# Performance work log

Measured on AMD Instinct MI355X. Metric: run time of the kernel, lower is better.

## Reference

```python
import jax, jax.numpy as jnp
import numpy as np

TEMP = 0.07
BASE_TEMP = 0.07
NUM_HEADS = 8


def setup_inputs() -> dict:
    key = jax.random.key(0)
    k1, k2, k3 = jax.random.split(key, 3)
    B, B2, V, E, C = 1024, 2048, 2, 512, 64
    features = jax.random.normal(k1, (B, V, E), dtype=jnp.float32)
    additional_negatives = jax.random.normal(k2, (B2, V, E), dtype=jnp.float32)
    labels = jax.random.bernoulli(k3, 0.05, (B, C)).astype(jnp.float32)
    return {"features": features, "additional_negatives": additional_negatives, "labels": labels}


def _l2norm(x, eps=1e-12):
    # matches torch.nn.functional.normalize (norm clamped at eps)
    n = jnp.linalg.norm(x, axis=-1, keepdims=True)
    return x / jnp.maximum(n, eps)


def reference(features, additional_negatives, labels):
    B, V, E = features.shape
    H = NUM_HEADS
    F = E // H
    N = B * V

    mask0 = (labels @ labels.T) > 0  # (B, B) label-overlap mask

    # torch.cat(torch.unbind(x, dim=1), dim=0): view-major concat -> (N, E)
    f = jnp.transpose(features, (1, 0, 2)).reshape(N, E).reshape(N, H, F)
    neg = jnp.transpose(additional_negatives, (1, 0, 2))
    M = neg.shape[0] * neg.shape[1]
    neg = neg.reshape(M, E // 1).reshape(M, H, F)

    f = _l2norm(f)
    neg = _l2norm(neg)

    # per-head pairwise similarities (the diagonal(dim1=2,dim2=3) of the full
    # (N,H,N,H) product keeps only matching heads -> einsum over shared h)
    D = jnp.einsum('ihf,jhf->ijh', f, f)      # (N, N, H)
    DN = jnp.einsum('ihf,mhf->imh', f, neg)   # (N, M, H)

    heads = jnp.argmax(D, axis=-1)            # (N, N) per-pair best head

    D = D / TEMP
    DN = DN / TEMP

    # The original builds L[i,k,j] = D[i,j,heads[i,k]]; its max over j and the
    # masked exp-sums depend only on (i, heads[i,k]), so compute per (i, h).
    m1 = jax.lax.stop_gradient(jnp.max(D, axis=1))   # (N, H) = max_j D[i,j,h]
    m2 = jax.lax.stop_gradient(jnp.max(DN, axis=1))  # (N, H) = max_m DN[i,m,h]

    not_self = 1.0 - jnp.eye(N, dtype=D.dtype)       # exclude j == i
    S1 = jnp.sum(jnp.exp(D - m1[:, None, :]) * not_self[:, :, None], axis=1)  # (N, H)
    S2 = jnp.sum(jnp.exp(DN - m2[:, None, :]), axis=1)                         # (N, H)

    # note: original sums exp terms referenced to DIFFERENT maxes (m1 vs m2);
    # reproduce that exactly.
    denom = m1 + jnp.log(S1 + S2)                    # (N, H)

    # diagonal term: D[i,k,heads[i,k]] == max_h D[i,k,h]
    Dmax = jnp.max(D, axis=-1)                       # (N, N)
    denom_ik = jnp.take_along_axis(denom, heads, axis=1)  # (N, N)
    log_prob = Dmax - denom_ik                       # (N, N)

    mask = jnp.tile(mask0, (V, V)).astype(D.dtype) * not_self  # (N, N)
    mean_log_prob_pos = jnp.sum(mask * log_prob, axis=1) / jnp.sum(mask, axis=1)
    loss_vec = -(TEMP / BASE_TEMP) * mean_log_prob_pos          # (N,)

    finite = jnp.isfinite(loss_vec)
    cnt = jnp.sum(finite.astype(loss_vec.dtype))
    loss = jnp.sum(jnp.where(finite, loss_vec, 0.0)) / cnt
    loss = jnp.where(jnp.isnan(loss), jnp.zeros((), loss.dtype), loss)
    return loss
```

## Files before the change

### kernel.cpp

```cpp
#include <hip/hip_runtime.h>

typedef unsigned long long u64;
typedef unsigned short ushort_t;
typedef __bf16 bf16x8 __attribute__((ext_vector_type(8)));
typedef float f32x4 __attribute__((ext_vector_type(4)));

#define NROWS 2048
#define MROWS 4096
#define BLAB  1024
#define INVT  (1.0f / 0.07f)
#define K2    (INVT * 1.4426950408889634f)

__device__ __forceinline__ bf16x8 ldb(const ushort_t* p) {
  return __builtin_bit_cast(bf16x8, *(const uint4*)p);
}

__device__ __forceinline__ ushort_t f2bf(float f) {
  unsigned u = __float_as_uint(f);
  u += 0x7fff + ((u >> 16) & 1);
  return (ushort_t)(u >> 16);
}

__global__ void k_prep(const float* __restrict__ feat, const float* __restrict__ negs,
                       const float* __restrict__ labels,
                       ushort_t* __restrict__ fnb, ushort_t* __restrict__ nnb,
                       u64* __restrict__ lbits, float* __restrict__ zbuf) {
  if (blockIdx.x >= 3072) {
    const int gtid = (blockIdx.x - 3072) * 256 + threadIdx.x;
    if (gtid < 4096) zbuf[gtid] = 0.0f;
    const int wid  = gtid >> 6;
    const int lane = threadIdx.x & 63;
    if (wid < BLAB) {
      float v = labels[wid * 64 + lane];
      u64 msk = __ballot(v != 0.0f);
      if (lane == 0) lbits[wid] = msk;
    }
    return;
  }
  const int wid  = blockIdx.x * 4 + ((threadIdx.x >> 6));
  const int lane = threadIdx.x & 63;
  const int g = lane >> 4, ln = lane & 15;
  const int p = wid * 4 + g;
  const float* src;
  ushort_t* dst;
  if (p < NROWS * 8) {
    const int i = p >> 3, h = p & 7;
    const int b = i & (BLAB - 1), v = i >> 10;
    src = feat + (b * 2 + v) * 512 + h * 64;
    dst = fnb + (h * NROWS + i) * 64;
  } else {
    const int q = p - NROWS * 8;
    const int m = q >> 3, h = q & 7;
    const int b2 = m & 2047, v = m >> 11;
    src = negs + (b2 * 2 + v) * 512 + h * 64;
    dst = nnb + (h * MROWS + m) * 64;
  }
  const float4 x = *(const float4*)(src + 4 * ln);
  float ss = x.x * x.x + x.y * x.y + x.z * x.z + x.w * x.w;
#pragma unroll
  for (int d = 1; d < 16; d <<= 1) ss += __shfl_xor(ss, d, 64);
  const float inv = 1.0f / fmaxf(sqrtf(ss), 1e-12f);
  ushort4 o;
  o.x = f2bf(x.x * inv); o.y = f2bf(x.y * inv);
  o.z = f2bf(x.z * inv); o.w = f2bf(x.w * inv);
  *(ushort4*)(dst + 4 * ln) = o;
}

__device__ __forceinline__ void store_ms4(float mc[4][4], float sa[4][4],
                                          float* __restrict__ gm, float* __restrict__ gs,
                                          int base, int off, int lg, int ln) {
#pragma unroll
  for (int rs = 0; rs < 4; ++rs) {
#pragma unroll
    for (int q = 0; q < 4; ++q) {
      float m = mc[rs][q], s = sa[rs][q];
#pragma unroll
      for (int d = 1; d < 16; d <<= 1) {
        m = fmaxf(m, __shfl_xor(m, d, 64));
        s += __shfl_xor(s, d, 64);
      }
      if (ln == 0) {
        const int row = base + rs * 16 + lg * 4 + q;
        gm[row * 128 + off] = m * INVT;
        gs[row * 128 + off] = s * exp2f((1.0f - m) * K2);
      }
      mc[rs][q] = -3.0e38f; sa[rs][q] = 0.0f;
    }
  }
}

__global__ __launch_bounds__(256, 2) void k_passA(const ushort_t* __restrict__ fnb,
                                                  const ushort_t* __restrict__ nnb,
                                                  float* __restrict__ m1p, float* __restrict__ S1p,
                                                  float* __restrict__ m2p, float* __restrict__ S2p) {
  const int tid  = threadIdx.x;
  const int head = blockIdx.x & 7;
  const int rbk  = (blockIdx.x >> 3) & 7;
  const int js   = blockIdx.x >> 6;
  const int w = tid >> 6, lane = tid & 63, lg = lane >> 4, ln = lane & 15;
  const ushort_t* fh = fnb + head * (NROWS * 64);
  const ushort_t* nh = nnb + head * (MROWS * 64);
  const int base = rbk * 256 + w * 64;
  const int off  = head * 16 + js;

  bf16x8 a0[4], a1[4];
#pragma unroll
  for (int rs = 0; rs < 4; ++rs) {
    const ushort_t* ap = fh + (base + rs * 16 + ln) * 64 + lg * 8;
    a0[rs] = ldb(ap); a1[rs] = ldb(ap + 32);
  }
  float mc[4][4], sa[4][4];
#pragma unroll
  for (int rs = 0; rs < 4; ++rs)
#pragma unroll
    for (int q = 0; q < 4; ++q) { mc[rs][q] = -3.0e38f; sa[rs][q] = 0.0f; }

  const int j0 = js * 128;
  const int t0 = js * 256;

  uint4 rb0 = *(const uint4*)(fh + (j0 + ln) * 64 + lg * 8);
  uint4 rb1 = *(const uint4*)(fh + (j0 + ln) * 64 + 32 + lg * 8);
  for (int ji = 0; ji < 8; ++ji) {
    const int j = j0 + ji * 16;
    const ushort_t* nsrc = (ji < 7) ? (fh + (j + 16 + ln) * 64) : (nh + (t0 + ln) * 64);
    const uint4 nb0 = *(const uint4*)(nsrc + lg * 8);
    const uint4 nb1 = *(const uint4*)(nsrc + 32 + lg * 8);
    const int gj = j + ln;
#pragma unroll
    for (int rs = 0; rs < 4; ++rs) {
      f32x4 c = {0.0f, 0.0f, 0.0f, 0.0f};
      c = __builtin_amdgcn_mfma_f32_16x16x32_bf16(a0[rs], __builtin_bit_cast(bf16x8, rb0), c, 0, 0, 0);
      c = __builtin_amdgcn_mfma_f32_16x16x32_bf16(a1[rs], __builtin_bit_cast(bf16x8, rb1), c, 0, 0, 0);
#pragma unroll
      for (int q = 0; q < 4; ++q) {
        const float cv = c[q];
        mc[rs][q] = fmaxf(mc[rs][q], cv);
        float e = exp2f(fmaf(cv, K2, -K2));
        if (base + rs * 16 + lg * 4 + q == gj) e = 0.0f;
        sa[rs][q] += e;
      }
    }
    rb0 = nb0; rb1 = nb1;
  }
  store_ms4(mc, sa, m1p, S1p, base, off, lg, ln);

  for (int ti = 0; ti < 16; ++ti) {
    const int t = t0 + ti * 16;
    const ushort_t* nsrc = nh + (((ti < 15) ? (t + 16) : t0) + ln) * 64;
    const uint4 nb0 = *(const uint4*)(nsrc + lg * 8);
    const uint4 nb1 = *(const uint4*)(nsrc + 32 + lg * 8);
#pragma unroll
    for (int rs = 0; rs < 4; ++rs) {
      f32x4 c = {0.0f, 0.0f, 0.0f, 0.0f};
      c = __builtin_amdgcn_mfma_f32_16x16x32_bf16(a0[rs], __builtin_bit_cast(bf16x8, rb0), c, 0, 0, 0);
      c = __builtin_amdgcn_mfma_f32_16x16x32_bf16(a1[rs], __builtin_bit_cast(bf16x8, rb1), c, 0, 0, 0);
#pragma unroll
      for (int q = 0; q < 4; ++q) {
        const float cv = c[q];
        mc[rs][q] = fmaxf(mc[rs][q], cv);
        sa[rs][q] += exp2f(fmaf(cv, K2, -K2));
      }
    }
    rb0 = nb0; rb1 = nb1;
  }
  store_ms4(mc, sa, m2p, S2p, base, off, lg, ln);
}

__global__ __launch_bounds__(256, 2) void k_passB(const ushort_t* __restrict__ fnb,
                                                  const float* __restrict__ m1p, const float* __restrict__ S1p,
                                                  const float* __restrict__ m2p, const float* __restrict__ S2p,
                                                  const u64* __restrict__ lbits,
                                                  float* __restrict__ rowsum, float* __restrict__ rowcnt) {
  __shared__ float dn[64 * 9];
  const int tid = threadIdx.x;
  const int it = blockIdx.x >> 5, jt = blockIdx.x & 31;
  const int ibase = it * 64, jbase = jt * 64;
  const int w = tid >> 6, lane = tid & 63, lg = lane >> 4, ln = lane & 15;

  for (int e = tid; e < 512; e += 256) {
    const int il = e >> 3, h = e & 7;
    const int bidx = (ibase + il) * 128 + h * 16;
    float4 mq[4], sq[4], m2q[4], s2q[4];
#pragma unroll
    for (int k = 0; k < 4; ++k) {
      mq[k]  = *(const float4*)(m1p + bidx + 4 * k);
      sq[k]  = *(const float4*)(S1p + bidx + 4 * k);
      m2q[k] = *(const float4*)(m2p + bidx + 4 * k);
      s2q[k] = *(const float4*)(S2p + bidx + 4 * k);
    }
    float m = -3.0e38f, m2 = -3.0e38f;
#pragma unroll
    for (int k = 0; k < 4; ++k) {
      m  = fmaxf(m,  fmaxf(fmaxf(mq[k].x,  mq[k].y),  fmaxf(mq[k].z,  mq[k].w)));
      m2 = fmaxf(m2, fmaxf(fmaxf(m2q[k].x, m2q[k].y), fmaxf(m2q[k].z, m2q[k].w)));
    }
    float s = 0.0f, s2 = 0.0f;
#pragma unroll
    for (int k = 0; k < 4; ++k) {
      s  += sq[k].x  * __expf(mq[k].x  - m)  + sq[k].y  * __expf(mq[k].y  - m)
          + sq[k].z  * __expf(mq[k].z  - m)  + sq[k].w  * __expf(mq[k].w  - m);
      s2 += s2q[k].x * __expf(m2q[k].x - m2) + s2q[k].y * __expf(m2q[k].y - m2)
          + s2q[k].z * __expf(m2q[k].z - m2) + s2q[k].w * __expf(m2q[k].w - m2);
    }
    dn[il * 9 + h] = m + __logf(s + s2);
  }
  __syncthreads();

  float dnr[4][8];
#pragma unroll
  for (int q = 0; q < 4; ++q) {
    const int il = w * 16 + lg * 4 + q;
#pragma unroll
    for (int h = 0; h < 8; ++h) dnr[q][h] = dn[il * 9 + h];
  }

  const int irow = ibase + w * 16 + ln;
  float maxd[4][4], bestdn[4][4];
#pragma unroll
  for (int sj = 0; sj < 4; ++sj)
#pragma unroll
    for (int q = 0; q < 4; ++q) { maxd[sj][q] = -3.0e38f; bestdn[sj][q] = 0.0f; }

#pragma unroll
  for (int h = 0; h < 8; ++h) {
    const ushort_t* fh = fnb + h * (NROWS * 64);
    const bf16x8 a0 = ldb(fh + irow * 64 + lg * 8);
    const bf16x8 a1 = ldb(fh + irow * 64 + 32 + lg * 8);
#pragma unroll
    for (int sj = 0; sj < 4; ++sj) {
      const int jrow = jbase + sj * 16 + ln;
      const bf16x8 b0 = ldb(fh + jrow * 64 + lg * 8);
      const bf16x8 b1 = ldb(fh + jrow * 64 + 32 + lg * 8);
      f32x4 c = {0.0f, 0.0f, 0.0f, 0.0f};
      c = __builtin_amdgcn_mfma_f32_16x16x32_bf16(a0, b0, c, 0, 0, 0);
      c = __builtin_amdgcn_mfma_f32_16x16x32_bf16(a1, b1, c, 0, 0, 0);
#pragma unroll
      for (int q = 0; q < 4; ++q)
        if (c[q] > maxd[sj][q]) { maxd[sj][q] = c[q]; bestdn[sj][q] = dnr[q][h]; }
    }
  }

  u64 lbi[4];
#pragma unroll
  for (int q = 0; q < 4; ++q) lbi[q] = lbits[(ibase + w * 16 + lg * 4 + q) & (BLAB - 1)];
  float rs[4] = {0, 0, 0, 0}, rc[4] = {0, 0, 0, 0};
#pragma unroll
  for (int sj = 0; sj < 4; ++sj) {
    const int gj = jbase + sj * 16 + ln;
    const u64 lbj = lbits[gj & (BLAB - 1)];
#pragma unroll
    for (int q = 0; q < 4; ++q) {
      const int gi = ibase + w * 16 + lg * 4 + q;
      if (gi != gj && (lbi[q] & lbj)) {
        rs[q] += maxd[sj][q] * INVT - bestdn[sj][q];
        rc[q] += 1.0f;
      }
    }
  }
#pragma unroll
  for (int q = 0; q < 4; ++q) {
#pragma unroll
    for (int d = 1; d < 16; d <<= 1) {
      rs[q] += __shfl_xor(rs[q], d, 64);
      rc[q] += __shfl_xor(rc[q], d, 64);
    }
  }
  if (ln == 0) {
#pragma unroll
    for (int q = 0; q < 4; ++q) {
      const int row = ibase + w * 16 + lg * 4 + q;
      atomicAdd(&rowsum[row], rs[q]);
      atomicAdd(&rowcnt[row], rc[q]);
    }
  }
}

__global__ void k_final(const float* __restrict__ rowsum, const float* __restrict__ rowcnt,
                        float* __restrict__ out) {
  __shared__ float sdata[4][2];
  const int tid = threadIdx.x;
  float s = 0.0f, c = 0.0f;
  for (int i = tid; i < NROWS; i += 256) {
    const float cnt = rowcnt[i];
    if (cnt > 0.0f) { s -= rowsum[i] / cnt; c += 1.0f; }
  }
#pragma unroll
  for (int d = 32; d; d >>= 1) { s += __shfl_xor(s, d, 64); c += __shfl_xor(c, d, 64); }
  const int w = tid >> 6;
  if ((tid & 63) == 0) { sdata[w][0] = s; sdata[w][1] = c; }
  __syncthreads();
  if (tid == 0) {
    s = 0.0f; c = 0.0f;
#pragma unroll
    for (int w2 = 0; w2 < 4; ++w2) { s += sdata[w2][0]; c += sdata[w2][1]; }
    out[0] = (c > 0.0f) ? s / c : 0.0f;
  }
}

extern "C" void kernel_launch(void* const* d_in, const int* in_sizes, int n_in,
                              void* d_out, int out_size, void* d_ws, size_t ws_size,
                              hipStream_t stream) {
  const float* feat   = (const float*)d_in[0];
  const float* negs   = (const float*)d_in[1];
  const float* labels = (const float*)d_in[2];
  float* out = (float*)d_out;

  ushort_t* fnb = (ushort_t*)d_ws;
  ushort_t* nnb = fnb + 8 * NROWS * 64;
  float* m1p = (float*)(nnb + 8 * MROWS * 64);
  float* S1p = m1p + NROWS * 128;
  float* m2p = S1p + NROWS * 128;
  float* S2p = m2p + NROWS * 128;
  float* rowsum = S2p + NROWS * 128;
  float* rowcnt = rowsum + 2048;
  u64*   lbits  = (u64*)(rowcnt + 2048);

  k_prep<<<3328, 256, 0, stream>>>(feat, negs, labels, fnb, nnb, lbits, rowsum);
  k_passA<<<1024, 256, 0, stream>>>(fnb, nnb, m1p, S1p, m2p, S2p);
  k_passB<<<1024, 256, 0, stream>>>(fnb, m1p, S1p, m2p, S2p, lbits, rowsum, rowcnt);
  k_final<<<1, 256, 0, stream>>>(rowsum, rowcnt, out);
}
```

Before: 173.6 us.

## Double-buffer passA tile loads and hoist denominator merge into separate kernel

In passA, the single-tile register prefetch becomes a two-deep register pipeline. Tiles are fetched two steps ahead, with the positive and negative loops sharing one stream of tile pointers, to hide more global load latency behind the MFMA and exp work. The per-row, per-head denominator merge over the 16 partial max/sum slices moves out of passB into a small k_denom kernel. Before, each of the 32 passB blocks sharing a row tile recomputed it. This adds one kernel launch and raises register pressure in passA, which could hurt occupancy under launch_bounds(256,2).

New measurement: 163.6 us. -5.8%, faster.

```diff
diff --git a/kernel.cpp b/kernel.cpp
--- a/kernel.cpp
+++ b/kernel.cpp
@@ -102,6 +102,8 @@
   const ushort_t* nh = nnb + head * (MROWS * 64);
   const int base = rbk * 256 + w * 64;
   const int off  = head * 16 + js;
+  const int j0 = js * 128;
+  const int t0 = js * 256;
 
   bf16x8 a0[4], a1[4];
 #pragma unroll
@@ -115,60 +117,99 @@
 #pragma unroll
     for (int q = 0; q < 4; ++q) { mc[rs][q] = -3.0e38f; sa[rs][q] = 0.0f; }
 
-  const int j0 = js * 128;
-  const int t0 = js * 256;
-
-  uint4 rb0 = *(const uint4*)(fh + (j0 + ln) * 64 + lg * 8);
-  uint4 rb1 = *(const uint4*)(fh + (j0 + ln) * 64 + 32 + lg * 8);
-  for (int ji = 0; ji < 8; ++ji) {
-    const int j = j0 + ji * 16;
-    const ushort_t* nsrc = (ji < 7) ? (fh + (j + 16 + ln) * 64) : (nh + (t0 + ln) * 64);
-    const uint4 nb0 = *(const uint4*)(nsrc + lg * 8);
-    const uint4 nb1 = *(const uint4*)(nsrc + 32 + lg * 8);
-    const int gj = j + ln;
-#pragma unroll
-    for (int rs = 0; rs < 4; ++rs) {
-      f32x4 c = {0.0f, 0.0f, 0.0f, 0.0f};
-      c = __builtin_amdgcn_mfma_f32_16x16x32_bf16(a0[rs], __builtin_bit_cast(bf16x8, rb0), c, 0, 0, 0);
-      c = __builtin_amdgcn_mfma_f32_16x16x32_bf16(a1[rs], __builtin_bit_cast(bf16x8, rb1), c, 0, 0, 0);
-#pragma unroll
-      for (int q = 0; q < 4; ++q) {
-        const float cv = c[q];
-        mc[rs][q] = fmaxf(mc[rs][q], cv);
-        float e = exp2f(fmaf(cv, K2, -K2));
-        if (base + rs * 16 + lg * 4 + q == gj) e = 0.0f;
-        sa[rs][q] += e;
-      }
-    }
-    rb0 = nb0; rb1 = nb1;
+#define TPTR(tt) ((tt) < 8 ? fh + (j0 + (tt) * 16 + ln) * 64 : nh + (t0 + ((tt) - 8) * 16 + ln) * 64)
+
+#define STEP(Pa, Pb, gjb, SELF)                                                              \
+  {                                                                                          \
+    _Pragma("unroll") for (int rs = 0; rs < 4; ++rs) {                                       \
+      f32x4 c = {0.0f, 0.0f, 0.0f, 0.0f};                                                    \
+      c = __builtin_amdgcn_mfma_f32_16x16x32_bf16(a0[rs], __builtin_bit_cast(bf16x8, Pa), c, 0, 0, 0); \
+      c = __builtin_amdgcn_mfma_f32_16x16x32_bf16(a1[rs], __builtin_bit_cast(bf16x8, Pb), c, 0, 0, 0); \
+      _Pragma("unroll") for (int q = 0; q < 4; ++q) {                                        \
+        const float cv = c[q];                                                               \
+        mc[rs][q] = fmaxf(mc[rs][q], cv);                                                    \
+        float e = exp2f(fmaf(cv, K2, -K2));                                                  \
+        if (SELF && (base + rs * 16 + lg * 4 + q == (gjb) + ln)) e = 0.0f;                   \
+        sa[rs][q] += e;                                                                      \
+      }                                                                                      \
+    }                                                                                        \
+  }
+
+  const ushort_t* p0 = TPTR(0);
+  uint4 P0a = *(const uint4*)(p0 + lg * 8), P0b = *(const uint4*)(p0 + 32 + lg * 8);
+  const ushort_t* p1 = TPTR(1);
+  uint4 P1a = *(const uint4*)(p1 + lg * 8), P1b = *(const uint4*)(p1 + 32 + lg * 8);
+
+  for (int ji = 0; ji < 8; ji += 2) {
+    {
+      const ushort_t* np = TPTR(ji + 2);
+      const uint4 na = *(const uint4*)(np + lg * 8), nb = *(const uint4*)(np + 32 + lg * 8);
+      STEP(P0a, P0b, j0 + ji * 16, 1);
+      P0a = na; P0b = nb;
+    }
+    {
+      const ushort_t* np = TPTR(ji + 3);
+      const uint4 na = *(const uint4*)(np + lg * 8), nb = *(const uint4*)(np + 32 + lg * 8);
+      STEP(P1a, P1b, j0 + (ji + 1) * 16, 1);
+      P1a = na; P1b = nb;
+    }
   }
   store_ms4(mc, sa, m1p, S1p, base, off, lg, ln);
 
-  for (int ti = 0; ti < 16; ++ti) {
-    const int t = t0 + ti * 16;
-    const ushort_t* nsrc = nh + (((ti < 15) ? (t + 16) : t0) + ln) * 64;
-    const uint4 nb0 = *(const uint4*)(nsrc + lg * 8);
-    const uint4 nb1 = *(const uint4*)(nsrc + 32 + lg * 8);
-#pragma unroll
-    for (int rs = 0; rs < 4; ++rs) {
-      f32x4 c = {0.0f, 0.0f, 0.0f, 0.0f};
-      c = __builtin_amdgcn_mfma_f32_16x16x32_bf16(a0[rs], __builtin_bit_cast(bf16x8, rb0), c, 0, 0, 0);
-      c = __builtin_amdgcn_mfma_f32_16x16x32_bf16(a1[rs], __builtin_bit_cast(bf16x8, rb1), c, 0, 0, 0);
-#pragma unroll
-      for (int q = 0; q < 4; ++q) {
-        const float cv = c[q];
-        mc[rs][q] = fmaxf(mc[rs][q], cv);
-        sa[rs][q] += exp2f(fmaf(cv, K2, -K2));
-      }
-    }
-    rb0 = nb0; rb1 = nb1;
+  for (int k = 0; k < 16; k += 2) {
+    {
+      const int tn = (k + 10 < 24) ? k + 10 : 23;
+      const ushort_t* np = TPTR(tn);
+      const uint4 na = *(const uint4*)(np + lg * 8), nb = *(const uint4*)(np + 32 + lg * 8);
+      STEP(P0a, P0b, 0, 0);
+      P0a = na; P0b = nb;
+    }
+    {
+      const int tn = (k + 11 < 24) ? k + 11 : 23;
+      const ushort_t* np = TPTR(tn);
+      const uint4 na = *(const uint4*)(np + lg * 8), nb = *(const uint4*)(np + 32 + lg * 8);
+      STEP(P1a, P1b, 0, 0);
+      P1a = na; P1b = nb;
+    }
   }
   store_ms4(mc, sa, m2p, S2p, base, off, lg, ln);
+#undef STEP
+#undef TPTR
+}
+
+__global__ void k_denom(const float* __restrict__ m1p, const float* __restrict__ S1p,
+                        const float* __restrict__ m2p, const float* __restrict__ S2p,
+                        float* __restrict__ dnm) {
+  const int e = blockIdx.x * 256 + threadIdx.x;
+  const int row = e >> 3, h = e & 7;
+  const int bidx = row * 128 + h * 16;
+  float4 mq[4], sq[4], m2q[4], s2q[4];
+#pragma unroll
+  for (int k = 0; k < 4; ++k) {
+    mq[k]  = *(const float4*)(m1p + bidx + 4 * k);
+    sq[k]  = *(const float4*)(S1p + bidx + 4 * k);
+    m2q[k] = *(const float4*)(m2p + bidx + 4 * k);
+    s2q[k] = *(const float4*)(S2p + bidx + 4 * k);
+  }
+  float m = -3.0e38f, m2 = -3.0e38f;
+#pragma unroll
+  for (int k = 0; k < 4; ++k) {
+    m  = fmaxf(m,  fmaxf(fmaxf(mq[k].x,  mq[k].y),  fmaxf(mq[k].z,  mq[k].w)));
+    m2 = fmaxf(m2, fmaxf(fmaxf(m2q[k].x, m2q[k].y), fmaxf(m2q[k].z, m2q[k].w)));
+  }
+  float s = 0.0f, s2 = 0.0f;
+#pragma unroll
+  for (int k = 0; k < 4; ++k) {
+    s  += sq[k].x  * __expf(mq[k].x  - m)  + sq[k].y  * __expf(mq[k].y  - m)
+        + sq[k].z  * __expf(mq[k].z  - m)  + sq[k].w  * __expf(mq[k].w  - m);
+    s2 += s2q[k].x * __expf(m2q[k].x - m2) + s2q[k].y * __expf(m2q[k].y - m2)
+        + s2q[k].z * __expf(m2q[k].z - m2) + s2q[k].w * __expf(m2q[k].w - m2);
+  }
+  dnm[row * 8 + h] = m + __logf(s + s2);
 }
 
 __global__ __launch_bounds__(256, 2) void k_passB(const ushort_t* __restrict__ fnb,
-                                                  const float* __restrict__ m1p, const float* __restrict__ S1p,
-                                                  const float* __restrict__ m2p, const float* __restrict__ S2p,
+                                                  const float* __restrict__ dnm,
                                                   const u64* __restrict__ lbits,
                                                   float* __restrict__ rowsum, float* __restrict__ rowcnt) {
   __shared__ float dn[64 * 9];
@@ -179,30 +220,7 @@
 
   for (int e = tid; e < 512; e += 256) {
     const int il = e >> 3, h = e & 7;
-    const int bidx = (ibase + il) * 128 + h * 16;
-    float4 mq[4], sq[4], m2q[4], s2q[4];
-#pragma unroll
-    for (int k = 0; k < 4; ++k) {
-      mq[k]  = *(const float4*)(m1p + bidx + 4 * k);
-      sq[k]  = *(const float4*)(S1p + bidx + 4 * k);
-      m2q[k] = *(const float4*)(m2p + bidx + 4 * k);
-      s2q[k] = *(const float4*)(S2p + bidx + 4 * k);
-    }
-    float m = -3.0e38f, m2 = -3.0e38f;
-#pragma unroll
-    for (int k = 0; k < 4; ++k) {
-      m  = fmaxf(m,  fmaxf(fmaxf(mq[k].x,  mq[k].y),  fmaxf(mq[k].z,  mq[k].w)));
-      m2 = fmaxf(m2, fmaxf(fmaxf(m2q[k].x, m2q[k].y), fmaxf(m2q[k].z, m2q[k].w)));
-    }
-    float s = 0.0f, s2 = 0.0f;
-#pragma unroll
-    for (int k = 0; k < 4; ++k) {
-      s  += sq[k].x  * __expf(mq[k].x  - m)  + sq[k].y  * __expf(mq[k].y  - m)
-          + sq[k].z  * __expf(mq[k].z  - m)  + sq[k].w  * __expf(mq[k].w  - m);
-      s2 += s2q[k].x * __expf(m2q[k].x - m2) + s2q[k].y * __expf(m2q[k].y - m2)
-          + s2q[k].z * __expf(m2q[k].z - m2) + s2q[k].w * __expf(m2q[k].w - m2);
-    }
-    dn[il * 9 + h] = m + __logf(s + s2);
+    dn[il * 9 + h] = dnm[(ibase + il) * 8 + h];
   }
   __syncthreads();
 
@@ -314,9 +332,11 @@
   float* rowsum = S2p + NROWS * 128;
   float* rowcnt = rowsum + 2048;
   u64*   lbits  = (u64*)(rowcnt + 2048);
+  float* dnm    = (float*)(lbits + 1024);
 
   k_prep<<<3328, 256, 0, stream>>>(feat, negs, labels, fnb, nnb, lbits, rowsum);
   k_passA<<<1024, 256, 0, stream>>>(fnb, nnb, m1p, S1p, m2p, S2p);
-  k_passB<<<1024, 256, 0, stream>>>(fnb, m1p, S1p, m2p, S2p, lbits, rowsum, rowcnt);
+  k_denom<<<64, 256, 0, stream>>>(m1p, S1p, m2p, S2p, dnm);
+  k_passB<<<1024, 256, 0, stream>>>(fnb, dnm, lbits, rowsum, rowcnt);
   k_final<<<1, 256, 0, stream>>>(rowsum, rowcnt, out);
 }
```
